# Kernel tuning notes

Hardware: AMD Instinct MI355X
Metric: run time of the kernel (lower is better)

## Reference

```python
import jax, jax.numpy as jnp
import numpy as np

N = 100000
IN_F, C1, C2, C3, OUT_F = 64, 64, 64, 64, 8


def setup_inputs() -> dict:
    key = jax.random.key(0)
    ks = jax.random.split(key, 12)
    x = jax.random.normal(ks[0], (N, IN_F), dtype=jnp.float32)
    edge_index = jax.random.randint(ks[1], (2, 1600000), 0, N, dtype=jnp.int64)

    def lin(kw, kb, fi, fo):
        s = 1.0 / np.sqrt(fi)
        W = jax.random.uniform(kw, (fi, fo), jnp.float32, -s, s)
        b = jax.random.uniform(kb, (fo,), jnp.float32, -s, s)
        return W, b

    W1, b1 = lin(ks[2], ks[3], IN_F, C1)
    W2, b2 = lin(ks[4], ks[5], C1, C2)
    W3, b3 = lin(ks[6], ks[7], C2, C3)
    Wl, bl = lin(ks[8], ks[9], C3, OUT_F)
    return {"x": x, "edge_index": edge_index, "W1": W1, "b1": b1,
            "W2": W2, "b2": b2, "W3": W3, "b3": b3, "Wl": Wl, "bl": bl}


def _gcn_norm(edge_index, n):
    # add self loops, compute symmetric normalization D^-1/2 A D^-1/2
    loops = jnp.arange(n, dtype=edge_index.dtype)
    src = jnp.concatenate([edge_index[0], loops])
    dst = jnp.concatenate([edge_index[1], loops])
    deg = jax.ops.segment_sum(jnp.ones_like(dst, dtype=jnp.float32), dst, num_segments=n)
    dis = jnp.where(deg > 0, jax.lax.rsqrt(deg), 0.0)
    norm = dis[src] * dis[dst]  # [E+N]
    return src, dst, norm


def _gcn_layer(h, W, b, src, dst, norm, n):
    h = h @ W                                   # [N, Fout] small GEMM
    msg = h[src] * norm[:, None]                # gather + scale, [E+N, Fout]
    agg = jax.ops.segment_sum(msg, dst, num_segments=n)  # scatter-add
    return agg + b


def reference(x, edge_index, W1, b1, W2, b2, W3, b3, Wl, bl):
    n = x.shape[0]
    src, dst, norm = _gcn_norm(edge_index, n)
    h = jax.nn.relu(_gcn_layer(x, W1, b1, src, dst, norm, n))
    h = jax.nn.relu(_gcn_layer(h, W2, b2, src, dst, norm, n))
    h = jax.nn.relu(_gcn_layer(h, W3, b3, src, dst, norm, n))
    return h @ Wl + bl
```

## Files before the change

### kernel.cpp

```cpp
#include <hip/hip_runtime.h>
#include <hip/hip_fp16.h>

#define F 64
#define CHUNK 2048
#define BN 512
#define BSHIFT 9
#define CAP 20480

typedef int v4i __attribute__((ext_vector_type(4)));

__device__ __forceinline__ float rlane(float v, int l) {
    return __uint_as_float(__builtin_amdgcn_readlane(__float_as_uint(v), l));
}

__global__ __launch_bounds__(256) void k_blkcnt(const int* __restrict__ dst,
                                                int* __restrict__ blkcnt,
                                                int E, int NB, int NBKT) {
    __shared__ int lcnt[256];
    int b = blockIdx.x, t = threadIdx.x;
    lcnt[t] = 0;
    __syncthreads();
    int e0 = b * CHUNK;
#pragma unroll
    for (int k = 0; k < 8; ++k) {
        int e = e0 + t + k * 256;
        if (e < E) {
            int d = __builtin_nontemporal_load(&dst[e]);
            atomicAdd(&lcnt[d >> BSHIFT], 1);
        }
    }
    __syncthreads();
    if (t < NBKT) blkcnt[t * NB + b] = lcnt[t];
}

__global__ __launch_bounds__(256) void k_bktscan(const int* __restrict__ blkcnt,
                                                 int* __restrict__ blkoff,
                                                 int* __restrict__ bkttot, int NB) {
    __shared__ int s[256];
    __shared__ int running;
    int seg = blockIdx.x;
    int t = threadIdx.x;
    if (t == 0) running = 0;
    __syncthreads();
    for (int base = 0; base < NB; base += 256) {
        int i = base + t;
        int v = (i < NB) ? blkcnt[seg * NB + i] : 0;
        s[t] = v;
        __syncthreads();
        for (int off = 1; off < 256; off <<= 1) {
            int x = (t >= off) ? s[t - off] : 0;
            __syncthreads();
            s[t] += x;
            __syncthreads();
        }
        int rbase = running;
        if (i < NB) blkoff[seg * NB + i] = rbase + s[t] - v;
        int ctot = s[255];
        __syncthreads();
        if (t == 0) running = rbase + ctot;
        __syncthreads();
    }
    if (t == 0) bkttot[seg] = running;
}

__global__ void k_sb(const int* __restrict__ bkttot, int* __restrict__ sb, int NBKT) {
    __shared__ int s[256];
    int t = threadIdx.x;
    int v = (t < NBKT) ? bkttot[t] : 0;
    s[t] = v;
    __syncthreads();
    for (int off = 1; off < 256; off <<= 1) {
        int x = (t >= off) ? s[t - off] : 0;
        __syncthreads();
        s[t] += x;
        __syncthreads();
    }
    if (t < NBKT) sb[t] = s[t] - v;
    if (t == NBKT - 1) sb[NBKT] = s[t];
}

__global__ __launch_bounds__(256) void k_stage2(const int* __restrict__ src,
                                                const int* __restrict__ dst,
                                                const int* __restrict__ blkoff,
                                                const int* __restrict__ sb,
                                                unsigned* __restrict__ stage,
                                                int E, int NB, int NBKT) {
    __shared__ int lcnt[256];
    __shared__ int lbase[257];
    __shared__ int obase[256];
    __shared__ int s[256];
    __shared__ unsigned rec[CHUNK];
    __shared__ unsigned char binof[CHUNK];
    int b = blockIdx.x, t = threadIdx.x;
    lcnt[t] = 0;
    __syncthreads();
    int e0 = b * CHUNK;
    int myseg[8], myrank[8];
    unsigned myrec[8];
#pragma unroll
    for (int k = 0; k < 8; ++k) {
        int e = e0 + t + k * 256;
        myseg[k] = -1;
        if (e < E) {
            int d = __builtin_nontemporal_load(&dst[e]);
            int sv = __builtin_nontemporal_load(&src[e]);
            int sg = d >> BSHIFT;
            myseg[k] = sg;
            myrank[k] = atomicAdd(&lcnt[sg], 1);
            myrec[k] = ((unsigned)(d & (BN - 1)) << 17) | (unsigned)sv;
        }
    }
    __syncthreads();
    int v = lcnt[t];
    s[t] = v;
    __syncthreads();
    for (int off = 1; off < 256; off <<= 1) {
        int x = (t >= off) ? s[t - off] : 0;
        __syncthreads();
        s[t] += x;
        __syncthreads();
    }
    lbase[t] = s[t] - v;
    if (t == 255) lbase[256] = s[255];
    obase[t] = (t < NBKT) ? sb[t] + blkoff[t * NB + b] : 0;
    __syncthreads();
#pragma unroll
    for (int k = 0; k < 8; ++k) {
        if (myseg[k] >= 0) {
            int p = lbase[myseg[k]] + myrank[k];
            rec[p] = myrec[k];
            binof[p] = (unsigned char)myseg[k];
        }
    }
    __syncthreads();
    int tot = lbase[256];
    for (int j = t; j < tot; j += 256) {
        int sg = binof[j];
        stage[obase[sg] + (j - lbase[sg])] = rec[j];
    }
}

__global__ __launch_bounds__(1024) void k_bincount(const unsigned* __restrict__ stage,
                                                   const int* __restrict__ sb,
                                                   int* __restrict__ count, int n) {
    __shared__ int lc[BN];
    int bkt = blockIdx.x, t = threadIdx.x;
    int nb0 = bkt << BSHIFT;
    for (int q = t; q < BN; q += 1024) lc[q] = 0;
    __syncthreads();
    int r0 = sb[bkt], r1 = sb[bkt + 1];
    for (int j = r0 + t; j < r1; j += 1024) {
        unsigned r = stage[j];
        atomicAdd(&lc[r >> 17], 1);
    }
    __syncthreads();
    for (int q = t; q < BN; q += 1024) {
        int node = nb0 + q;
        if (node < n) count[node] = lc[q];
    }
}

__global__ void k_reduce(const int* __restrict__ c, int* __restrict__ bsum, int n) {
    __shared__ int s[256];
    int t = threadIdx.x;
    int i = blockIdx.x * 256 + t;
    s[t] = (i < n) ? ((c[i] + 3) & ~3) : 0;
    __syncthreads();
    for (int off = 128; off > 0; off >>= 1) {
        if (t < off) s[t] += s[t + off];
        __syncthreads();
    }
    if (t == 0) bsum[blockIdx.x] = s[0];
}

__global__ void k_scan_bsum(int* bs, int nb) {
    __shared__ int s[512];
    int t = threadIdx.x;
    int v = (t < nb) ? bs[t] : 0;
    s[t] = v;
    __syncthreads();
    for (int off = 1; off < 512; off <<= 1) {
        int x = (t >= off) ? s[t - off] : 0;
        __syncthreads();
        s[t] += x;
        __syncthreads();
    }
    if (t < nb) bs[t] = s[t] - v;
}

__global__ void k_scan_write(const int* __restrict__ c, const int* __restrict__ boff,
                             int* __restrict__ row_start, float* __restrict__ dis, int n) {
    __shared__ int s[256];
    int t = threadIdx.x;
    int i = blockIdx.x * 256 + t;
    int cv = (i < n) ? c[i] : 0;
    int v = (cv + 3) & ~3;
    if (i >= n) v = 0;
    s[t] = v;
    __syncthreads();
    for (int off = 1; off < 256; off <<= 1) {
        int x = (t >= off) ? s[t - off] : 0;
        __syncthreads();
        s[t] += x;
        __syncthreads();
    }
    if (i <= n) {
        row_start[i] = s[t] - v + boff[blockIdx.x];
        if (i < n) dis[i] = rsqrtf((float)(cv + 1));
    }
}

__global__ __launch_bounds__(256) void k_binfill(const unsigned* __restrict__ stage,
                                                 const int* __restrict__ sb,
                                                 const int* __restrict__ row_start,
                                                 int* __restrict__ csr, int n) {
    __shared__ int lcur[BN];
    __shared__ int buf[CAP];
    int bkt = blockIdx.x, t = threadIdx.x;
    int nb0 = bkt << BSHIFT;
    int nend = min(nb0 + BN, n);
    int w0 = row_start[nb0];
    int w1 = row_start[nend];
    int wlen = w1 - w0;
    for (int j = t; j < wlen && j < CAP; j += 256) buf[j] = n;
    for (int q = t; q < BN; q += 256) {
        int node = nb0 + q;
        lcur[q] = (node < nend) ? row_start[node] - w0 : 0;
    }
    __syncthreads();
    int r0 = sb[bkt], r1 = sb[bkt + 1];
    for (int j = r0 + t; j < r1; j += 256) {
        unsigned r = stage[j];
        int p = atomicAdd(&lcur[r >> 17], 1);
        if (p < CAP) buf[p] = (int)(r & 0x1FFFFu);
    }
    __syncthreads();
    for (int j = t; j < wlen && j < CAP; j += 256) csr[w0 + j] = buf[j];
}

__global__ void k_prep(const float4* __restrict__ x4, const float* __restrict__ dis,
                       uint2* __restrict__ hs, uint2* __restrict__ hs2, int n) {
    int i = blockIdx.x * blockDim.x + threadIdx.x;
    int tot = (n + 1) * 16;
    if (i < tot) {
        int row = i >> 4;
        float dv = 0.0f;
        float4 v = make_float4(0.f, 0.f, 0.f, 0.f);
        if (row < n) { dv = dis[row]; v = x4[i]; }
        __half2 h01 = __floats2half2_rn(dv * v.x, dv * v.y);
        __half2 h23 = __floats2half2_rn(dv * v.z, dv * v.w);
        uint2 u;
        u.x = *(unsigned*)&h01;
        u.y = *(unsigned*)&h23;
        hs[i] = u;
    } else if (i < tot + 16) {
        hs2[(size_t)n * 16 + (i - tot)] = make_uint2(0u, 0u);
    }
}

__device__ __forceinline__ void h4acc(uint2 u, float* t) {
    float2 fa = __half22float2(*(__half2*)&u.x);
    float2 fb = __half22float2(*(__half2*)&u.y);
    t[0] += fa.x; t[1] += fa.y; t[2] += fb.x; t[3] += fb.y;
}

__global__ __launch_bounds__(256) void k_layer(const __half* __restrict__ hin,
                                               const float* __restrict__ W,
                                               const float* __restrict__ b,
                                               const int* __restrict__ row_start,
                                               const int* __restrict__ csr,
                                               const float* __restrict__ dis,
                                               __half* __restrict__ hout,
                                               int n, int scale_out) {
    __shared__ float Ws[F * F];
    int tid = threadIdx.x;
#pragma unroll
    for (int i = 0; i < 16; ++i) Ws[tid + i * 256] = W[tid + i * 256];
    __syncthreads();
    int lane = tid & 63;
    int g = lane >> 4;
    int sub = lane & 15;
    int r0 = (blockIdx.x * 4 + (tid >> 6)) * 4;
    if (r0 >= n) return;

    int s0 = row_start[r0];
    int s1 = row_start[r0 + 1];
    int s2 = row_start[r0 + 2];
    int s3 = row_start[r0 + 3];
    int s4 = row_start[r0 + 4];

    float a0[4] = {0, 0, 0, 0};
    float a1[4] = {0, 0, 0, 0};
    float a2[4] = {0, 0, 0, 0};
    float a3[4] = {0, 0, 0, 0};

    const v4i* csr4 = (const v4i*)csr;
    const uint2* h2 = (const uint2*)hin;
    int B0 = s0 >> 2, B4 = s4 >> 2;

    auto ldidx = [&](int bb) -> v4i {
        int mybb = bb + g;
        bool valid = mybb < B4;
        v4i qq = __builtin_nontemporal_load(csr4 + (valid ? mybb : B0));
        if (!valid) { qq.x = n; qq.y = n; qq.z = n; qq.w = n; }
        return qq;
    };

    if (B0 < B4) {
        v4i qcur = ldidx(B0);
        v4i qnxt = (B0 + 4 < B4) ? ldidx(B0 + 4) : qcur;
        uint2 Gc0 = h2[((size_t)qcur.x << 4) + sub];
        uint2 Gc1 = h2[((size_t)qcur.y << 4) + sub];
        uint2 Gc2 = h2[((size_t)qcur.z << 4) + sub];
        uint2 Gc3 = h2[((size_t)qcur.w << 4) + sub];

        for (int bb = B0; bb < B4; bb += 4) {
            bool hasn = bb + 4 < B4;
            uint2 Gn0, Gn1, Gn2, Gn3;
            if (hasn) {
                Gn0 = h2[((size_t)qnxt.x << 4) + sub];
                Gn1 = h2[((size_t)qnxt.y << 4) + sub];
                Gn2 = h2[((size_t)qnxt.z << 4) + sub];
                Gn3 = h2[((size_t)qnxt.w << 4) + sub];
            }
            v4i qn2 = (bb + 8 < B4) ? ldidx(bb + 8) : qnxt;

            int slot = (bb + g) << 2;
            int r = (slot >= s1) + ((slot >= s2) + (slot >= s3));
            float t[4] = {0, 0, 0, 0};
            h4acc(Gc0, t); h4acc(Gc1, t); h4acc(Gc2, t); h4acc(Gc3, t);
            float m0 = (r == 0) ? 1.0f : 0.0f;
            float m1 = (r == 1) ? 1.0f : 0.0f;
            float m2 = (r == 2) ? 1.0f : 0.0f;
            float m3 = (r == 3) ? 1.0f : 0.0f;
#pragma unroll
            for (int m = 0; m < 4; ++m) {
                a0[m] = fmaf(m0, t[m], a0[m]);
                a1[m] = fmaf(m1, t[m], a1[m]);
                a2[m] = fmaf(m2, t[m], a2[m]);
                a3[m] = fmaf(m3, t[m], a3[m]);
            }
            qnxt = qn2;
            if (hasn) { Gc0 = Gn0; Gc1 = Gn1; Gc2 = Gn2; Gc3 = Gn3; }
        }
    }

#pragma unroll
    for (int m = 0; m < 4; ++m) {
        a0[m] += __shfl_xor(a0[m], 16); a0[m] += __shfl_xor(a0[m], 32);
        a1[m] += __shfl_xor(a1[m], 16); a1[m] += __shfl_xor(a1[m], 32);
        a2[m] += __shfl_xor(a2[m], 16); a2[m] += __shfl_xor(a2[m], 32);
        a3[m] += __shfl_xor(a3[m], 16); a3[m] += __shfl_xor(a3[m], 32);
    }

    {
        uint2 u0 = h2[((size_t)(r0 + 0) << 4) + sub];
        uint2 u1 = h2[((size_t)(r0 + 1) << 4) + sub];
        uint2 u2 = h2[((size_t)(r0 + 2) << 4) + sub];
        uint2 u3 = h2[((size_t)(r0 + 3) << 4) + sub];
        h4acc(u0, a0); h4acc(u1, a1); h4acc(u2, a2); h4acc(u3, a3);
    }
    float d0 = dis[r0 + 0], d1 = dis[r0 + 1], d2 = dis[r0 + 2], d3 = dis[r0 + 3];
#pragma unroll
    for (int m = 0; m < 4; ++m) {
        a0[m] *= d0; a1[m] *= d1; a2[m] *= d2; a3[m] *= d3;
    }

    float bb_ = b[lane];
    float y0 = bb_, y1 = bb_, y2 = bb_, y3 = bb_;
#pragma unroll
    for (int a = 0; a < 16; ++a) {
#pragma unroll
        for (int m = 0; m < 4; ++m) {
            float w = Ws[(((a << 2) + m) << 6) + lane];
            y0 = fmaf(rlane(a0[m], a), w, y0);
            y1 = fmaf(rlane(a1[m], a), w, y1);
            y2 = fmaf(rlane(a2[m], a), w, y2);
            y3 = fmaf(rlane(a3[m], a), w, y3);
        }
    }
    y0 = fmaxf(y0, 0.0f);
    y1 = fmaxf(y1, 0.0f);
    y2 = fmaxf(y2, 0.0f);
    y3 = fmaxf(y3, 0.0f);
    if (scale_out) { y0 *= d0; y1 *= d1; y2 *= d2; y3 *= d3; }
    hout[((size_t)(r0 + 0) << 6) + lane] = __float2half(y0);
    hout[((size_t)(r0 + 1) << 6) + lane] = __float2half(y1);
    hout[((size_t)(r0 + 2) << 6) + lane] = __float2half(y2);
    hout[((size_t)(r0 + 3) << 6) + lane] = __float2half(y3);
}

__global__ __launch_bounds__(256) void k_final(const __half* __restrict__ h,
                                               const float* __restrict__ Wl,
                                               const float* __restrict__ bl,
                                               float* __restrict__ out, int n) {
    __shared__ float Ws[F * 8];
    __shared__ float bs[8];
    int tid = threadIdx.x;
    Ws[tid] = Wl[tid];
    Ws[tid + 256] = Wl[tid + 256];
    if (tid < 8) bs[tid] = bl[tid];
    __syncthreads();
    int idx = blockIdx.x * 256 + tid;
    if (idx >= n * 8) return;
    int row = idx >> 3;
    int o = idx & 7;
    const __half* hr = h + (size_t)row * F;
    float acc = bs[o];
#pragma unroll
    for (int k = 0; k < F; ++k) acc = fmaf(__half2float(hr[k]), Ws[k * 8 + o], acc);
    out[idx] = acc;
}

extern "C" void kernel_launch(void* const* d_in, const int* in_sizes, int n_in,
                              void* d_out, int out_size, void* d_ws, size_t ws_size,
                              hipStream_t stream) {
    const float* x  = (const float*)d_in[0];
    const int*   ei = (const int*)d_in[1];
    const float* W1 = (const float*)d_in[2];
    const float* b1 = (const float*)d_in[3];
    const float* W2 = (const float*)d_in[4];
    const float* b2 = (const float*)d_in[5];
    const float* W3 = (const float*)d_in[6];
    const float* b3 = (const float*)d_in[7];
    const float* Wl = (const float*)d_in[8];
    const float* bl = (const float*)d_in[9];
    float* out = (float*)d_out;

    int n = in_sizes[0] / F;
    int E = in_sizes[1] / 2;
    const int* src = ei;
    const int* dst = ei + E;

    int np   = (n + 256) & ~255;
    int nb   = (np + 255) / 256;
    int cap  = E + 3 * n + 64;
    int NB   = (E + CHUNK - 1) / CHUNK;
    int NBKT = (n + BN - 1) >> BSHIFT;

    int*      count     = (int*)d_ws;
    int*      row_start = count + np;
    int*      bsum      = row_start + np;
    int*      blkcnt    = bsum + 512;
    int*      blkoff    = blkcnt + 256 * NB;
    int*      bkttot    = blkoff + 256 * NB;
    int*      sb        = bkttot + 256;
    float*    dis       = (float*)(sb + 272);
    unsigned* stage     = (unsigned*)(dis + np);
    int*      csr       = (int*)(stage + ((E + 3) & ~3));
    __half*   buf1      = (__half*)(csr + ((cap + 3) & ~3));
    __half*   buf2      = buf1 + (size_t)(n + 1) * F;

    k_blkcnt<<<NB, 256, 0, stream>>>(dst, blkcnt, E, NB, NBKT);

    k_bktscan<<<NBKT, 256, 0, stream>>>(blkcnt, blkoff, bkttot, NB);
    k_sb<<<1, 256, 0, stream>>>(bkttot, sb, NBKT);
    k_stage2<<<NB, 256, 0, stream>>>(src, dst, blkoff, sb, stage, E, NB, NBKT);

    k_bincount<<<NBKT, 1024, 0, stream>>>(stage, sb, count, n);

    k_reduce<<<nb, 256, 0, stream>>>(count, bsum, n);
    k_scan_bsum<<<1, 512, 0, stream>>>(bsum, nb);
    k_scan_write<<<nb, 256, 0, stream>>>(count, bsum, row_start, dis, n);

    k_binfill<<<NBKT, 256, 0, stream>>>(stage, sb, row_start, csr, n);

    k_prep<<<((n + 1) * 16 + 16 + 255) / 256, 256, 0, stream>>>(
        (const float4*)x, dis, (uint2*)buf1, (uint2*)buf2, n);

    int nb_l = (n / 4 + 3) / 4;
    k_layer<<<nb_l, 256, 0, stream>>>(buf1, W1, b1, row_start, csr, dis, buf2, n, 1);
    k_layer<<<nb_l, 256, 0, stream>>>(buf2, W2, b2, row_start, csr, dis, buf1, n, 1);
    k_layer<<<nb_l, 256, 0, stream>>>(buf1, W3, b3, row_start, csr, dis, buf2, n, 0);

    k_final<<<(n * 8 + 255) / 256, 256, 0, stream>>>(buf2, Wl, bl, out, n);
}
```

Baseline: 314.6 us.

## Fold CSR prefix scan into bincount and binfill kernels, drop three launches

The separate reduce, block-sum scan and scan-write kernels are replaced. Bincount now also writes dis and a per-bucket padded total, a single small kernel scans the bucket totals, and binfill computes the per-node exclusive scan within its bucket and writes row_start itself. This cuts the number of launches and global passes over the count array in the CSR build, at the cost of a serial 512-wide shared-memory scan inside binfill and a wider binfill block.

Result: faster. 293.8 us (-6.6%).

```diff
diff --git a/kernel.cpp b/kernel.cpp
--- a/kernel.cpp
+++ b/kernel.cpp
@@ -142,11 +142,13 @@
 
 __global__ __launch_bounds__(1024) void k_bincount(const unsigned* __restrict__ stage,
                                                    const int* __restrict__ sb,
-                                                   int* __restrict__ count, int n) {
+                                                   int* __restrict__ count,
+                                                   float* __restrict__ dis,
+                                                   int* __restrict__ padtot, int n) {
     __shared__ int lc[BN];
     int bkt = blockIdx.x, t = threadIdx.x;
     int nb0 = bkt << BSHIFT;
-    for (int q = t; q < BN; q += 1024) lc[q] = 0;
+    if (t < BN) lc[t] = 0;
     __syncthreads();
     int r0 = sb[bkt], r1 = sb[bkt + 1];
     for (int j = r0 + t; j < r1; j += 1024) {
@@ -154,48 +156,31 @@
         atomicAdd(&lc[r >> 17], 1);
     }
     __syncthreads();
-    for (int q = t; q < BN; q += 1024) {
-        int node = nb0 + q;
-        if (node < n) count[node] = lc[q];
-    }
-}
-
-__global__ void k_reduce(const int* __restrict__ c, int* __restrict__ bsum, int n) {
+    int pv = 0;
+    if (t < BN) {
+        int node = nb0 + t;
+        int cv = lc[t];
+        if (node < n) {
+            count[node] = cv;
+            dis[node] = rsqrtf((float)(cv + 1));
+            pv = (cv + 3) & ~3;
+        }
+    }
+    __syncthreads();
+    if (t < BN) lc[t] = pv;
+    __syncthreads();
+    for (int off = 256; off > 0; off >>= 1) {
+        if (t < off) lc[t] += lc[t + off];
+        __syncthreads();
+    }
+    if (t == 0) padtot[bkt] = lc[0];
+}
+
+__global__ void k_sb2(const int* __restrict__ padtot, int* __restrict__ rbase,
+                      int* __restrict__ row_start, int NBKT, int n) {
     __shared__ int s[256];
     int t = threadIdx.x;
-    int i = blockIdx.x * 256 + t;
-    s[t] = (i < n) ? ((c[i] + 3) & ~3) : 0;
-    __syncthreads();
-    for (int off = 128; off > 0; off >>= 1) {
-        if (t < off) s[t] += s[t + off];
-        __syncthreads();
-    }
-    if (t == 0) bsum[blockIdx.x] = s[0];
-}
-
-__global__ void k_scan_bsum(int* bs, int nb) {
-    __shared__ int s[512];
-    int t = threadIdx.x;
-    int v = (t < nb) ? bs[t] : 0;
-    s[t] = v;
-    __syncthreads();
-    for (int off = 1; off < 512; off <<= 1) {
-        int x = (t >= off) ? s[t - off] : 0;
-        __syncthreads();
-        s[t] += x;
-        __syncthreads();
-    }
-    if (t < nb) bs[t] = s[t] - v;
-}
-
-__global__ void k_scan_write(const int* __restrict__ c, const int* __restrict__ boff,
-                             int* __restrict__ row_start, float* __restrict__ dis, int n) {
-    __shared__ int s[256];
-    int t = threadIdx.x;
-    int i = blockIdx.x * 256 + t;
-    int cv = (i < n) ? c[i] : 0;
-    int v = (cv + 3) & ~3;
-    if (i >= n) v = 0;
+    int v = (t < NBKT) ? padtot[t] : 0;
     s[t] = v;
     __syncthreads();
     for (int off = 1; off < 256; off <<= 1) {
@@ -204,38 +189,46 @@
         s[t] += x;
         __syncthreads();
     }
-    if (i <= n) {
-        row_start[i] = s[t] - v + boff[blockIdx.x];
-        if (i < n) dis[i] = rsqrtf((float)(cv + 1));
-    }
-}
-
-__global__ __launch_bounds__(256) void k_binfill(const unsigned* __restrict__ stage,
+    if (t < NBKT) rbase[t] = s[t] - v;
+    if (t == NBKT - 1) { rbase[NBKT] = s[t]; row_start[n] = s[t]; }
+}
+
+__global__ __launch_bounds__(512) void k_binfill(const unsigned* __restrict__ stage,
                                                  const int* __restrict__ sb,
-                                                 const int* __restrict__ row_start,
+                                                 const int* __restrict__ count,
+                                                 const int* __restrict__ rbase,
+                                                 int* __restrict__ row_start,
                                                  int* __restrict__ csr, int n) {
     __shared__ int lcur[BN];
+    __shared__ int sc[BN];
     __shared__ int buf[CAP];
     int bkt = blockIdx.x, t = threadIdx.x;
     int nb0 = bkt << BSHIFT;
-    int nend = min(nb0 + BN, n);
-    int w0 = row_start[nb0];
-    int w1 = row_start[nend];
-    int wlen = w1 - w0;
-    for (int j = t; j < wlen && j < CAP; j += 256) buf[j] = n;
-    for (int q = t; q < BN; q += 256) {
-        int node = nb0 + q;
-        lcur[q] = (node < nend) ? row_start[node] - w0 : 0;
-    }
+    int node = nb0 + t;
+    int pv = (node < n) ? ((count[node] + 3) & ~3) : 0;
+    sc[t] = pv;
+    __syncthreads();
+    for (int off = 1; off < BN; off <<= 1) {
+        int x = (t >= off) ? sc[t - off] : 0;
+        __syncthreads();
+        sc[t] += x;
+        __syncthreads();
+    }
+    int excl = sc[t] - pv;
+    int w0 = rbase[bkt];
+    int wlen = sc[BN - 1];
+    lcur[t] = excl;
+    if (node < n) row_start[node] = w0 + excl;
+    for (int j = t; j < wlen && j < CAP; j += 512) buf[j] = n;
     __syncthreads();
     int r0 = sb[bkt], r1 = sb[bkt + 1];
-    for (int j = r0 + t; j < r1; j += 256) {
+    for (int j = r0 + t; j < r1; j += 512) {
         unsigned r = stage[j];
         int p = atomicAdd(&lcur[r >> 17], 1);
         if (p < CAP) buf[p] = (int)(r & 0x1FFFFu);
     }
     __syncthreads();
-    for (int j = t; j < wlen && j < CAP; j += 256) csr[w0 + j] = buf[j];
+    for (int j = t; j < wlen && j < CAP; j += 512) csr[w0 + j] = buf[j];
 }
 
 __global__ void k_prep(const float4* __restrict__ x4, const float* __restrict__ dis,
@@ -433,19 +426,19 @@
     const int* dst = ei + E;
 
     int np   = (n + 256) & ~255;
-    int nb   = (np + 255) / 256;
     int cap  = E + 3 * n + 64;
     int NB   = (E + CHUNK - 1) / CHUNK;
     int NBKT = (n + BN - 1) >> BSHIFT;
 
     int*      count     = (int*)d_ws;
     int*      row_start = count + np;
-    int*      bsum      = row_start + np;
-    int*      blkcnt    = bsum + 512;
+    int*      blkcnt    = row_start + np;
     int*      blkoff    = blkcnt + 256 * NB;
     int*      bkttot    = blkoff + 256 * NB;
     int*      sb        = bkttot + 256;
-    float*    dis       = (float*)(sb + 272);
+    int*      padtot    = sb + 272;
+    int*      rbase     = padtot + 256;
+    float*    dis       = (float*)(rbase + 272);
     unsigned* stage     = (unsigned*)(dis + np);
     int*      csr       = (int*)(stage + ((E + 3) & ~3));
     __half*   buf1      = (__half*)(csr + ((cap + 3) & ~3));
@@ -457,13 +450,10 @@
     k_sb<<<1, 256, 0, stream>>>(bkttot, sb, NBKT);
     k_stage2<<<NB, 256, 0, stream>>>(src, dst, blkoff, sb, stage, E, NB, NBKT);
 
-    k_bincount<<<NBKT, 1024, 0, stream>>>(stage, sb, count, n);
-
-    k_reduce<<<nb, 256, 0, stream>>>(count, bsum, n);
-    k_scan_bsum<<<1, 512, 0, stream>>>(bsum, nb);
-    k_scan_write<<<nb, 256, 0, stream>>>(count, bsum, row_start, dis, n);
-
-    k_binfill<<<NBKT, 256, 0, stream>>>(stage, sb, row_start, csr, n);
+    k_bincount<<<NBKT, 1024, 0, stream>>>(stage, sb, count, dis, padtot, n);
+    k_sb2<<<1, 256, 0, stream>>>(padtot, rbase, row_start, NBKT, n);
+
+    k_binfill<<<NBKT, 512, 0, stream>>>(stage, sb, count, rbase, row_start, csr, n);
 
     k_prep<<<((n + 1) * 16 + 16 + 255) / 256, 256, 0, stream>>>(
         (const float4*)x, dis, (uint2*)buf1, (uint2*)buf2, n);
```
